# Optimization experiments

Measured on AMD Instinct MI355X. Metric: run time of the kernel, lower is better.

The kernel has to match this reference:

```python
import jax, jax.numpy as jnp
import numpy as np

N_NODES = 100000
N_EDGES = 640000
D_IN = 128
D_OUT = 128
BN_EPS = 1e-5


def setup_inputs() -> dict:
    key = jax.random.key(0)
    k1, k2, k3, k4 = jax.random.split(key, 4)
    x = jax.random.normal(k1, (N_NODES, D_IN), dtype=jnp.float32)
    edge_index = jax.random.randint(k2, (2, N_EDGES), 0, N_NODES, dtype=jnp.int64)
    W = jax.random.normal(k3, (D_IN, D_OUT), dtype=jnp.float32) * (1.0 / np.sqrt(D_IN))
    b = jnp.zeros((D_OUT,), dtype=jnp.float32)
    gamma = jnp.ones((D_OUT,), dtype=jnp.float32)
    beta = jnp.zeros((D_OUT,), dtype=jnp.float32)
    return {"x": x, "edge_index": edge_index, "W": W, "b": b, "gamma": gamma, "beta": beta}


def reference(x, edge_index, W, b, gamma, beta):
    N = x.shape[0]
    # --- GCNConv: add self-loops, symmetric normalization ---
    loop = jnp.arange(N, dtype=edge_index.dtype)
    src = jnp.concatenate([edge_index[0], loop])  # [E+N]
    dst = jnp.concatenate([edge_index[1], loop])  # [E+N]
    deg = jax.ops.segment_sum(jnp.ones_like(dst, dtype=x.dtype), dst, num_segments=N)
    dinv = jax.lax.rsqrt(deg)  # deg >= 1 due to self-loops
    norm = dinv[src] * dinv[dst]  # [E+N]
    # linear transform first (PyG order), then gather-normalize-scatter
    h = x @ W  # [N, D_OUT]
    msg = h[src] * norm[:, None]  # [E+N, D_OUT]
    agg = jax.ops.segment_sum(msg, dst, num_segments=N) + b  # [N, D_OUT]
    # --- ReLU ---
    r = jax.nn.relu(agg)
    # --- BatchNorm over node axis (training-mode batch statistics) ---
    mean = r.mean(axis=0)
    var = r.var(axis=0)
    out = gamma * (r - mean) * jax.lax.rsqrt(var + BN_EPS) + beta
    # dropout: identity in eval/deterministic mode
    return out
```

## Files before the change

kernel.cpp:

```cpp
#include <hip/hip_runtime.h>
#include <hip/hip_bf16.h>

#define N_NODES 100000
#define N_EDGES 640000
#define D 128
#define BN_EPS 1e-5f
#define NB_FILL 2500
#define NB_CVT 6250
#define NREP 64
#define BM 64
#define CS_LD 130
#define SLOTS 16
#define OSLOTS 32

typedef __attribute__((ext_vector_type(8))) short short8;
typedef __attribute__((ext_vector_type(4))) float f32x4;
typedef __attribute__((ext_vector_type(4))) unsigned int u32x4;

__device__ inline unsigned int f2bf(float f) {
    unsigned int u = __builtin_bit_cast(unsigned int, f);
    return (u + 0x7FFFu + ((u >> 16) & 1u)) >> 16;
}
__device__ inline float bflo(unsigned int p) { return __builtin_bit_cast(float, p << 16); }
__device__ inline float bfhi(unsigned int p) { return __builtin_bit_cast(float, p & 0xFFFF0000u); }

__global__ void k_zero(int* __restrict__ cnt, float* __restrict__ rep) {
    int i = blockIdx.x * 256 + threadIdx.x;
    if (i < N_NODES) cnt[i] = 0;
    if (i < NREP * 256) rep[i] = 0.0f;
}

__global__ __launch_bounds__(256) void k_prep(const int* __restrict__ ei, int* __restrict__ cnt,
                                              int* __restrict__ buck, int* __restrict__ buck2,
                                              const float* __restrict__ x, uint4* __restrict__ xb,
                                              const float* __restrict__ W,
                                              unsigned short* __restrict__ Wfrag) {
    const int bid = blockIdx.x;
    const int t = threadIdx.x;
    if (bid < NB_FILL) {
        const int e = bid * 256 + t;
        if (e < N_EDGES) {
            const int src = ei[e];
            const int d = ei[N_EDGES + e];
            const int slot = atomicAdd(&cnt[d], 1);
            if (slot < SLOTS)
                __builtin_nontemporal_store(src, &buck[(size_t)d * SLOTS + slot]);
            else if (slot < SLOTS + OSLOTS)
                __builtin_nontemporal_store(src, &buck2[(size_t)d * OSLOTS + slot - SLOTS]);
        }
    } else if (bid < NB_FILL + NB_CVT) {
        const size_t i = (size_t)(bid - NB_FILL) * 256 + t;
        const float4* xg = (const float4*)x;
        float4 a = xg[2 * i], c = xg[2 * i + 1];
        uint4 o;
        o.x = f2bf(a.x) | (f2bf(a.y) << 16);
        o.y = f2bf(a.z) | (f2bf(a.w) << 16);
        o.z = f2bf(c.x) | (f2bf(c.y) << 16);
        o.w = f2bf(c.z) | (f2bf(c.w) << 16);
        xb[i] = o;
    } else {
        const int i = (bid - NB_FILL - NB_CVT) * 256 + t;
        const int e  = i & 7;
        const int l  = (i >> 3) & 63;
        const int ct = (i >> 9) & 7;
        const int kk = i >> 12;
        const int lr = l & 15, lk = l >> 4;
        const int k   = kk * 32 + lk * 8 + e;
        const int col = ct * 16 + lr;
        Wfrag[i] = (unsigned short)f2bf(W[(size_t)k * D + col]);
    }
}

__global__ __launch_bounds__(1024) void k_gmm(const int* __restrict__ buck,
                                              const int* __restrict__ buck2,
                                              const int* __restrict__ cnt,
                                              const unsigned int* __restrict__ xb,
                                              const unsigned short* __restrict__ Wfrag,
                                              const float* __restrict__ b,
                                              unsigned int* __restrict__ outb,
                                              float* __restrict__ rep) {
    __shared__ __align__(16) char U[BM * CS_LD * 4];
    unsigned int* As_u = (unsigned int*)U;
    float* Cs = (float*)U;
    __shared__ float lsum[16][32];
    __shared__ float lsq[16][32];

    const int t = threadIdx.x;
    const int w = t >> 6;
    const int l = t & 63;
    const int lr = l & 15;
    const int lk = l >> 4;
    const int r0 = blockIdx.x * BM;

    for (int rr = 0; rr < 4; ++rr) {
        const int lrow = w * 4 + rr;
        int n = r0 + lrow; if (n >= N_NODES) n = N_NODES - 1;
        const int deg = cnt[n];
        const float di = rsqrtf((float)(deg + 1));
        const unsigned int hv = xb[(size_t)n * 64 + l];
        const float dd = di * di;
        float ax = bflo(hv) * dd;
        float ay = bfhi(hv) * dd;

        const int m = (deg > SLOTS + OSLOTS) ? (SLOTS + OSLOTS) : deg;
        int s_l = 0; float f_l = 0.0f;
        if (l < m) {
            s_l = (l < SLOTS) ? buck[(size_t)n * SLOTS + l]
                              : buck2[(size_t)n * OSLOTS + l - SLOTS];
            f_l = rsqrtf((float)(cnt[s_l] + 1)) * di;
        }
        for (int k = 0; k < m; k += 8) {
            unsigned int v[8];
            float f[8];
#pragma unroll
            for (int i = 0; i < 8; ++i) {
                const int sj = __builtin_amdgcn_readlane(s_l, k + i);
                f[i] = __builtin_bit_cast(float,
                    __builtin_amdgcn_readlane(__builtin_bit_cast(int, f_l), k + i));
                v[i] = xb[(size_t)sj * 64 + l];
            }
#pragma unroll
            for (int i = 0; i < 8; ++i) {
                ax = fmaf(bflo(v[i]), f[i], ax);
                ay = fmaf(bfhi(v[i]), f[i], ay);
            }
        }
        As_u[lrow * 64 + ((((l >> 2) ^ (lrow & 15)) << 2) | (l & 3))] =
            f2bf(ax) | (f2bf(ay) << 16);
    }
    __syncthreads();

    const int arow = (w & 3) * 16 + lr;
    const uint4* As4 = (const uint4*)U;
    short8 a[4];
#pragma unroll
    for (int kk = 0; kk < 4; ++kk)
        a[kk] = *(const short8*)&As4[arow * 16 + ((kk * 4 + lk) ^ (arow & 15))];
    __syncthreads();

    const int ct0 = (w >> 2) * 2;
    f32x4 acc[2];
    acc[0] = (f32x4)(0.0f);
    acc[1] = (f32x4)(0.0f);
#pragma unroll
    for (int kk = 0; kk < 4; ++kk) {
#pragma unroll
        for (int c = 0; c < 2; ++c) {
            const short8 bb = *(const short8*)(Wfrag + ((((kk * 8 + ct0 + c) << 6) + l) << 3));
            acc[c] = __builtin_amdgcn_mfma_f32_16x16x32_bf16(a[kk], bb, acc[c], 0, 0, 0);
        }
    }

    float s[2] = {0.0f, 0.0f}, s2[2] = {0.0f, 0.0f};
#pragma unroll
    for (int c = 0; c < 2; ++c) {
        const int ct = ct0 + c;
        const float bias = b[ct * 16 + lr];
#pragma unroll
        for (int r = 0; r < 4; ++r) {
            const int lrow = (w & 3) * 16 + lk * 4 + r;
            const float v = fmaxf(acc[c][r] + bias, 0.0f);
            if (r0 + lrow < N_NODES) {
                s[c] += v;
                s2[c] = fmaf(v, v, s2[c]);
            }
            Cs[lrow * CS_LD + ct * 16 + lr] = v;
        }
    }
#pragma unroll
    for (int c = 0; c < 2; ++c) {
        s[c]  += __shfl_xor(s[c], 16);  s[c]  += __shfl_xor(s[c], 32);
        s2[c] += __shfl_xor(s2[c], 16); s2[c] += __shfl_xor(s2[c], 32);
    }
    if (l < 16) {
#pragma unroll
        for (int c = 0; c < 2; ++c) {
            lsum[w][c * 16 + lr] = s[c];
            lsq[w][c * 16 + lr]  = s2[c];
        }
    }
    __syncthreads();

    {
        const int v = t;
        const int row = v >> 4;
        const int q   = v & 15;
        if (r0 + row < N_NODES) {
            const float* p = &Cs[row * CS_LD + q * 8];
            u32x4 o;
            o.x = f2bf(p[0]) | (f2bf(p[1]) << 16);
            o.y = f2bf(p[2]) | (f2bf(p[3]) << 16);
            o.z = f2bf(p[4]) | (f2bf(p[5]) << 16);
            o.w = f2bf(p[6]) | (f2bf(p[7]) << 16);
            __builtin_nontemporal_store(o, (u32x4*)outb + (size_t)(r0 + row) * 16 + q);
        }
    }

    if (t < 128) {
        const int g = t >> 5;
        const int cc = t & 31;
        const float ssum = lsum[4 * g + 0][cc] + lsum[4 * g + 1][cc]
                         + lsum[4 * g + 2][cc] + lsum[4 * g + 3][cc];
        const float ssq  = lsq[4 * g + 0][cc] + lsq[4 * g + 1][cc]
                         + lsq[4 * g + 2][cc] + lsq[4 * g + 3][cc];
        const int col = g * 32 + cc;
        float* r = rep + (blockIdx.x & (NREP - 1)) * 256;
        atomicAdd(&r[col],       ssum);
        atomicAdd(&r[128 + col], ssq);
    }
}

__global__ __launch_bounds__(256) void k_red(const float* __restrict__ rep,
                                             const float* __restrict__ gamma,
                                             const float* __restrict__ beta,
                                             float* __restrict__ sclsft) {
    __shared__ float sh[256];
    const int t = threadIdx.x;
    float s = 0.0f;
    for (int r = 0; r < NREP; ++r) s += rep[r * 256 + t];
    sh[t] = s;
    __syncthreads();
    if (t < 128) {
        const float inv_n = 1.0f / (float)N_NODES;
        const float mean = sh[t] * inv_n;
        const float var = sh[128 + t] * inv_n - mean * mean;
        const float sc = gamma[t] * rsqrtf(var + BN_EPS);
        sclsft[t]       = sc;
        sclsft[128 + t] = beta[t] - mean * sc;
    }
}

__global__ __launch_bounds__(256) void k_norm(const uint4* __restrict__ outb,
                                              float* __restrict__ out,
                                              const float* __restrict__ sclsft) {
    __shared__ float sc[256];
    const int t = threadIdx.x;
    sc[t] = sclsft[t];
    __syncthreads();
    const int i = blockIdx.x * 256 + t;
    if (i >= N_NODES * 16) return;
    const int c0 = (i & 15) * 8;
    const uint4 v = outb[i];
    f32x4 o0, o1;
    o0.x = fmaf(bflo(v.x), sc[c0 + 0], sc[128 + c0 + 0]);
    o0.y = fmaf(bfhi(v.x), sc[c0 + 1], sc[128 + c0 + 1]);
    o0.z = fmaf(bflo(v.y), sc[c0 + 2], sc[128 + c0 + 2]);
    o0.w = fmaf(bfhi(v.y), sc[c0 + 3], sc[128 + c0 + 3]);
    o1.x = fmaf(bflo(v.z), sc[c0 + 4], sc[128 + c0 + 4]);
    o1.y = fmaf(bfhi(v.z), sc[c0 + 5], sc[128 + c0 + 5]);
    o1.z = fmaf(bflo(v.w), sc[c0 + 6], sc[128 + c0 + 6]);
    o1.w = fmaf(bfhi(v.w), sc[c0 + 7], sc[128 + c0 + 7]);
    __builtin_nontemporal_store(o0, (f32x4*)out + (size_t)i * 2);
    __builtin_nontemporal_store(o1, (f32x4*)out + (size_t)i * 2 + 1);
}

extern "C" void kernel_launch(void* const* d_in, const int* in_sizes, int n_in,
                              void* d_out, int out_size, void* d_ws, size_t ws_size,
                              hipStream_t stream) {
    const float* x     = (const float*)d_in[0];
    const int*   ei    = (const int*)d_in[1];
    const float* W     = (const float*)d_in[2];
    const float* b     = (const float*)d_in[3];
    const float* gamma = (const float*)d_in[4];
    const float* beta  = (const float*)d_in[5];
    float* out = (float*)d_out;

    char* ws = (char*)d_ws;
    int*            cnt    = (int*)(ws + 0);
    float*          rep    = (float*)(ws + (512u << 10));
    float*          sclsft = (float*)(ws + (640u << 10));
    unsigned short* Wfrag  = (unsigned short*)(ws + (704u << 10));
    int*            buck   = (int*)(ws + (1024u << 10));
    int*            buck2  = (int*)(ws + (8192u << 10));
    unsigned int*   xb     = (unsigned int*)(ws + (24576u << 10));
    unsigned int*   outb   = (unsigned int*)(ws + (57344u << 10));

    k_zero<<<(N_NODES + 255) / 256, 256, 0, stream>>>(cnt, rep);
    k_prep<<<NB_FILL + NB_CVT + 64, 256, 0, stream>>>(ei, cnt, buck, buck2, x, (uint4*)xb,
                                                      W, Wfrag);
    k_gmm<<<(N_NODES + BM - 1) / BM, 1024, 0, stream>>>(buck, buck2, cnt, xb, Wfrag, b,
                                                        outb, rep);
    k_red<<<1, 256, 0, stream>>>(rep, gamma, beta, sclsft);
    k_norm<<<(N_NODES * 16 + 255) / 256, 256, 0, stream>>>((const uint4*)outb, out, sclsft);
}
```

Before: 125.7 us.

## Interleave edge bucketing with x conversion blocks and replace zero kernel with memset

Alternates edge-bucketing blocks with bf16 conversion blocks in the prep kernel so atomic-heavy and bandwidth-heavy work overlap on the GPU. Replaces the zeroing kernel with a hipMemsetAsync over a compacted workspace region, and switches nontemporal stores to regular stores for intermediates that are read again soon. The risk is that regular stores pollute cache and interleaving changes the atomic contention pattern.

```diff
diff --git a/kernel.cpp b/kernel.cpp
--- a/kernel.cpp
+++ b/kernel.cpp
@@ -15,7 +15,6 @@
 
 typedef __attribute__((ext_vector_type(8))) short short8;
 typedef __attribute__((ext_vector_type(4))) float f32x4;
-typedef __attribute__((ext_vector_type(4))) unsigned int u32x4;
 
 __device__ inline unsigned int f2bf(float f) {
     unsigned int u = __builtin_bit_cast(unsigned int, f);
@@ -23,12 +22,6 @@
 }
 __device__ inline float bflo(unsigned int p) { return __builtin_bit_cast(float, p << 16); }
 __device__ inline float bfhi(unsigned int p) { return __builtin_bit_cast(float, p & 0xFFFF0000u); }
-
-__global__ void k_zero(int* __restrict__ cnt, float* __restrict__ rep) {
-    int i = blockIdx.x * 256 + threadIdx.x;
-    if (i < N_NODES) cnt[i] = 0;
-    if (i < NREP * 256) rep[i] = 0.0f;
-}
 
 __global__ __launch_bounds__(256) void k_prep(const int* __restrict__ ei, int* __restrict__ cnt,
                                               int* __restrict__ buck, int* __restrict__ buck2,
@@ -37,27 +30,22 @@
                                               unsigned short* __restrict__ Wfrag) {
     const int bid = blockIdx.x;
     const int t = threadIdx.x;
-    if (bid < NB_FILL) {
-        const int e = bid * 256 + t;
-        if (e < N_EDGES) {
-            const int src = ei[e];
-            const int d = ei[N_EDGES + e];
-            const int slot = atomicAdd(&cnt[d], 1);
-            if (slot < SLOTS)
-                __builtin_nontemporal_store(src, &buck[(size_t)d * SLOTS + slot]);
-            else if (slot < SLOTS + OSLOTS)
-                __builtin_nontemporal_store(src, &buck2[(size_t)d * OSLOTS + slot - SLOTS]);
-        }
+    int xi = -1;
+    if (bid < 2 * NB_FILL) {
+        if (bid & 1) {
+            const int e = (bid >> 1) * 256 + t;
+            if (e < N_EDGES) {
+                const int src = ei[e];
+                const int d = ei[N_EDGES + e];
+                const int slot = atomicAdd(&cnt[d], 1);
+                if (slot < SLOTS) buck[(size_t)d * SLOTS + slot] = src;
+                else if (slot < SLOTS + OSLOTS) buck2[(size_t)d * OSLOTS + slot - SLOTS] = src;
+            }
+            return;
+        }
+        xi = bid >> 1;
     } else if (bid < NB_FILL + NB_CVT) {
-        const size_t i = (size_t)(bid - NB_FILL) * 256 + t;
-        const float4* xg = (const float4*)x;
-        float4 a = xg[2 * i], c = xg[2 * i + 1];
-        uint4 o;
-        o.x = f2bf(a.x) | (f2bf(a.y) << 16);
-        o.y = f2bf(a.z) | (f2bf(a.w) << 16);
-        o.z = f2bf(c.x) | (f2bf(c.y) << 16);
-        o.w = f2bf(c.z) | (f2bf(c.w) << 16);
-        xb[i] = o;
+        xi = bid - NB_FILL;
     } else {
         const int i = (bid - NB_FILL - NB_CVT) * 256 + t;
         const int e  = i & 7;
@@ -68,7 +56,17 @@
         const int k   = kk * 32 + lk * 8 + e;
         const int col = ct * 16 + lr;
         Wfrag[i] = (unsigned short)f2bf(W[(size_t)k * D + col]);
-    }
+        return;
+    }
+    const size_t i = (size_t)xi * 256 + t;
+    const float4* xg = (const float4*)x;
+    float4 a = xg[2 * i], c = xg[2 * i + 1];
+    uint4 o;
+    o.x = f2bf(a.x) | (f2bf(a.y) << 16);
+    o.y = f2bf(a.z) | (f2bf(a.w) << 16);
+    o.z = f2bf(c.x) | (f2bf(c.y) << 16);
+    o.w = f2bf(c.z) | (f2bf(c.w) << 16);
+    xb[i] = o;
 }
 
 __global__ __launch_bounds__(1024) void k_gmm(const int* __restrict__ buck,
@@ -182,17 +180,17 @@
     __syncthreads();
 
     {
-        const int v = t;
-        const int row = v >> 4;
-        const int q   = v & 15;
+        const int vv = t;
+        const int row = vv >> 4;
+        const int q   = vv & 15;
         if (r0 + row < N_NODES) {
             const float* p = &Cs[row * CS_LD + q * 8];
-            u32x4 o;
+            uint4 o;
             o.x = f2bf(p[0]) | (f2bf(p[1]) << 16);
             o.y = f2bf(p[2]) | (f2bf(p[3]) << 16);
             o.z = f2bf(p[4]) | (f2bf(p[5]) << 16);
             o.w = f2bf(p[6]) | (f2bf(p[7]) << 16);
-            __builtin_nontemporal_store(o, (u32x4*)outb + (size_t)(r0 + row) * 16 + q);
+            ((uint4*)outb)[(size_t)(r0 + row) * 16 + q] = o;
         }
     }
 
@@ -231,7 +229,7 @@
 }
 
 __global__ __launch_bounds__(256) void k_norm(const uint4* __restrict__ outb,
-                                              float* __restrict__ out,
+                                              float4* __restrict__ out,
                                               const float* __restrict__ sclsft) {
     __shared__ float sc[256];
     const int t = threadIdx.x;
@@ -241,7 +239,7 @@
     if (i >= N_NODES * 16) return;
     const int c0 = (i & 15) * 8;
     const uint4 v = outb[i];
-    f32x4 o0, o1;
+    float4 o0, o1;
     o0.x = fmaf(bflo(v.x), sc[c0 + 0], sc[128 + c0 + 0]);
     o0.y = fmaf(bfhi(v.x), sc[c0 + 1], sc[128 + c0 + 1]);
     o0.z = fmaf(bflo(v.y), sc[c0 + 2], sc[128 + c0 + 2]);
@@ -250,8 +248,8 @@
     o1.y = fmaf(bfhi(v.z), sc[c0 + 5], sc[128 + c0 + 5]);
     o1.z = fmaf(bflo(v.w), sc[c0 + 6], sc[128 + c0 + 6]);
     o1.w = fmaf(bfhi(v.w), sc[c0 + 7], sc[128 + c0 + 7]);
-    __builtin_nontemporal_store(o0, (f32x4*)out + (size_t)i * 2);
-    __builtin_nontemporal_store(o1, (f32x4*)out + (size_t)i * 2 + 1);
+    out[(size_t)i * 2]     = o0;
+    out[(size_t)i * 2 + 1] = o1;
 }
 
 extern "C" void kernel_launch(void* const* d_in, const int* in_sizes, int n_in,
@@ -267,19 +265,20 @@
 
     char* ws = (char*)d_ws;
     int*            cnt    = (int*)(ws + 0);
-    float*          rep    = (float*)(ws + (512u << 10));
-    float*          sclsft = (float*)(ws + (640u << 10));
-    unsigned short* Wfrag  = (unsigned short*)(ws + (704u << 10));
-    int*            buck   = (int*)(ws + (1024u << 10));
-    int*            buck2  = (int*)(ws + (8192u << 10));
-    unsigned int*   xb     = (unsigned int*)(ws + (24576u << 10));
-    unsigned int*   outb   = (unsigned int*)(ws + (57344u << 10));
-
-    k_zero<<<(N_NODES + 255) / 256, 256, 0, stream>>>(cnt, rep);
+    float*          rep    = (float*)(ws + 400000);
+    float*          sclsft = (float*)(ws + 466944);
+    unsigned short* Wfrag  = (unsigned short*)(ws + 468992);
+    int*            buck   = (int*)(ws + 1048576);
+    int*            buck2  = (int*)(ws + 8388608);
+    unsigned int*   xb     = (unsigned int*)(ws + 25165824);
+    unsigned int*   outb   = (unsigned int*)(ws + 58720256);
+
+    hipMemsetAsync(ws, 0, 465536, stream);
     k_prep<<<NB_FILL + NB_CVT + 64, 256, 0, stream>>>(ei, cnt, buck, buck2, x, (uint4*)xb,
                                                       W, Wfrag);
     k_gmm<<<(N_NODES + BM - 1) / BM, 1024, 0, stream>>>(buck, buck2, cnt, xb, Wfrag, b,
                                                         outb, rep);
     k_red<<<1, 256, 0, stream>>>(rep, gamma, beta, sclsft);
-    k_norm<<<(N_NODES * 16 + 255) / 256, 256, 0, stream>>>((const uint4*)outb, out, sclsft);
-}
+    k_norm<<<(N_NODES * 16 + 255) / 256, 256, 0, stream>>>((const uint4*)outb, (float4*)out,
+                                                           sclsft);
+}
```

Result: faster. 116.6 us (-7.3%).
